# Optimization experiments

Hardware: AMD Instinct MI355X
Metric: run time of the kernel (lower is better)

Reference implementation:

```python
import jax, jax.numpy as jnp
import numpy as np

EPS = 1e-12  # F.normalize default eps


def _l2norm(x, axis):
    n = jnp.sqrt(jnp.sum(x * x, axis=axis, keepdims=True))
    return x / jnp.maximum(n, EPS)


def setup_inputs() -> dict:
    key = jax.random.key(0)
    k1, k2, k3, k4 = jax.random.split(key, 4)
    N, T, C, K = 64, 577, 768, 64
    return {
        "grids": jax.random.normal(k1, (N, T, C), dtype=jnp.float32),
        "conv_w": jax.random.normal(k2, (K, C), dtype=jnp.float32) * 0.03,
        "conv_b": jax.random.normal(k3, (K,), dtype=jnp.float32) * 0.01,
        "centroids": jax.random.normal(k4, (K, C), dtype=jnp.float32) * 0.03,
    }


def reference(grids, conv_w, conv_b, centroids):
    # grids: (N, 577, 768) -> (N, C=768, T=577), matching view+permute in torch
    N = grids.shape[0]
    x = jnp.transpose(grids.reshape(N, 577, 768), (0, 2, 1))  # (N, C, T)
    # per-token L2 normalization over channel dim
    x = _l2norm(x, axis=1)
    # 1x1 conv == per-token linear: (N, K, T)
    logits = jnp.einsum('kc,nct->nkt', conv_w, x) + conv_b[None, :, None]
    a = jax.nn.softmax(logits, axis=1)  # softmax over regions K
    # NetVLAD algebraic rewrite of sum_t a[n,k,t]*(x[n,:,t]-c[k,:]):
    #   = (a @ x^T)[n,k,c] - sum_t(a)[n,k] * c[k,c]
    p = jnp.einsum('nkt,nct->nkc', a, x) - a.sum(axis=-1)[:, :, None] * centroids[None]
    p = _l2norm(p, axis=2)             # intra-region normalization
    p = p.reshape(N, -1)               # (N, K*C)
    p = _l2norm(p, axis=1)             # global normalization
    return p
```

## Files before the change

kernel.cpp:

```cpp
#include <hip/hip_runtime.h>
#include <math.h>

#define TT 577
#define TP 640
#define CCH 768
#define KR 64
#define NB 64

typedef __attribute__((ext_vector_type(8))) short bf16x8;
typedef __attribute__((ext_vector_type(8))) unsigned short ushort8;
typedef __attribute__((ext_vector_type(4))) float f32x4;

static constexpr float EPSF = 1e-12f;

static __device__ inline unsigned short f2bf(float f) {
    union { float f; unsigned int u; } v; v.f = f;
    unsigned int r = (v.u + 0x7FFFu + ((v.u >> 16) & 1u)) >> 16;
    return (unsigned short)r;
}
static __device__ inline float bf2f(unsigned short b) {
    union { unsigned int u; float f; } v; v.u = ((unsigned int)b) << 16;
    return v.f;
}

__global__ __launch_bounds__(256) void k_logits(
    const float* __restrict__ grids,
    const float* __restrict__ conv_w,
    const float* __restrict__ conv_b,
    unsigned short* __restrict__ ws_a,
    float* __restrict__ ws_norm)
{
    __shared__ __align__(16) unsigned short Wl[KR * 136];
    __shared__ __align__(16) unsigned short Abuf[4][KR * 24];

    const int tid  = threadIdx.x;
    const int lane = tid & 63;
    const int w    = tid >> 6;
    const int n    = blockIdx.x / 10;
    const int tb   = (blockIdx.x - n * 10) << 6;
    const int t0w  = tb + (w << 4);

    const int lr = lane & 15;
    const int lg = lane >> 4;

    const int tokA = t0w + lr;
    const bool validA = (tokA < TT);
    const float* gsrc = grids + ((size_t)n * TT + tokA) * CCH + (lg << 3);

    f32x4 acc[4] = {};
    float ss = 0.f;

    for (int c0 = 0; c0 < CCH; c0 += 128) {
        #pragma unroll
        for (int it = 0; it < 4; ++it) {
            int f = tid + (it << 8);
            int kr = f >> 4;
            int c8 = (f & 15) << 3;
            const float* src = conv_w + (size_t)kr * CCH + c0 + c8;
            float4 v0 = *reinterpret_cast<const float4*>(src);
            float4 v1 = *reinterpret_cast<const float4*>(src + 4);
            unsigned short* dst = &Wl[kr * 136 + c8];
            dst[0]=f2bf(v0.x); dst[1]=f2bf(v0.y); dst[2]=f2bf(v0.z); dst[3]=f2bf(v0.w);
            dst[4]=f2bf(v1.x); dst[5]=f2bf(v1.y); dst[6]=f2bf(v1.z); dst[7]=f2bf(v1.w);
        }
        __syncthreads();

        #pragma unroll
        for (int s = 0; s < 4; ++s) {
            float a8[8];
            if (validA) {
                float4 u0 = *reinterpret_cast<const float4*>(gsrc + c0 + (s << 5));
                float4 u1 = *reinterpret_cast<const float4*>(gsrc + c0 + (s << 5) + 4);
                a8[0]=u0.x; a8[1]=u0.y; a8[2]=u0.z; a8[3]=u0.w;
                a8[4]=u1.x; a8[5]=u1.y; a8[6]=u1.z; a8[7]=u1.w;
            } else {
                #pragma unroll
                for (int j = 0; j < 8; ++j) a8[j] = 0.f;
            }
            bf16x8 afrag;
            #pragma unroll
            for (int j = 0; j < 8; ++j) {
                ss = fmaf(a8[j], a8[j], ss);
                ((unsigned short*)&afrag)[j] = f2bf(a8[j]);
            }
            const int cl = (s << 5) + (lg << 3);
            #pragma unroll
            for (int rt = 0; rt < 4; ++rt) {
                bf16x8 bfrag = *reinterpret_cast<const bf16x8*>(&Wl[(rt*16 + lr)*136 + cl]);
                acc[rt] = __builtin_amdgcn_mfma_f32_16x16x32_bf16(afrag, bfrag, acc[rt], 0, 0, 0);
            }
        }
        __syncthreads();
    }

    ss += __shfl_xor(ss, 16);
    ss += __shfl_xor(ss, 32);
    const float nrm = sqrtf(ss);
    const float inv = 1.0f / fmaxf(nrm, EPSF);
    if (lane < 16) ws_norm[n * TP + t0w + lane] = nrm;

    float b_[4];
    #pragma unroll
    for (int rt = 0; rt < 4; ++rt) b_[rt] = conv_b[rt*16 + lr];

    float invT[4];
    #pragma unroll
    for (int reg = 0; reg < 4; ++reg) invT[reg] = __shfl(inv, (lg << 2) + reg);

    float lgt[4][4], mx[4];
    #pragma unroll
    for (int reg = 0; reg < 4; ++reg) {
        float m = -1e30f;
        #pragma unroll
        for (int rt = 0; rt < 4; ++rt) {
            lgt[rt][reg] = fmaf(acc[rt][reg], invT[reg], b_[rt]);
            m = fmaxf(m, lgt[rt][reg]);
        }
        mx[reg] = m;
    }
    #pragma unroll
    for (int msk = 1; msk < 16; msk <<= 1) {
        #pragma unroll
        for (int reg = 0; reg < 4; ++reg) mx[reg] = fmaxf(mx[reg], __shfl_xor(mx[reg], msk));
    }
    float ex[4][4], sm[4] = {0.f, 0.f, 0.f, 0.f};
    #pragma unroll
    for (int rt = 0; rt < 4; ++rt) {
        #pragma unroll
        for (int reg = 0; reg < 4; ++reg) {
            ex[rt][reg] = __expf(lgt[rt][reg] - mx[reg]);
            sm[reg] += ex[rt][reg];
        }
    }
    #pragma unroll
    for (int msk = 1; msk < 16; msk <<= 1) {
        #pragma unroll
        for (int reg = 0; reg < 4; ++reg) sm[reg] += __shfl_xor(sm[reg], msk);
    }

    #pragma unroll
    for (int reg = 0; reg < 4; ++reg) {
        const int trow = (lg << 2) + reg;
        const bool vt = (t0w + trow) < TT;
        const float scale = vt ? (invT[reg] / sm[reg]) : 0.f;
        #pragma unroll
        for (int rt = 0; rt < 4; ++rt)
            Abuf[w][(rt*16 + lr)*24 + trow] = f2bf(ex[rt][reg] * scale);
    }
    __syncthreads();

    {
        ushort8 r0 = *reinterpret_cast<const ushort8*>(&Abuf[w][lane * 24]);
        ushort8 r1 = *reinterpret_cast<const ushort8*>(&Abuf[w][lane * 24 + 8]);
        unsigned short* dst = ws_a + ((size_t)n * KR + lane) * TP + t0w;
        *reinterpret_cast<ushort8*>(dst)     = r0;
        *reinterpret_cast<ushort8*>(dst + 8) = r1;
    }
}

__global__ __launch_bounds__(256) void k_vlad(
    const float* __restrict__ grids,
    const unsigned short* __restrict__ ws_a,
    const float* __restrict__ ws_norm,
    const float* __restrict__ centroids,
    float* __restrict__ out)
{
    __shared__ __align__(16) unsigned short Gs[32 * 196];
    __shared__ float asum_red[4][64];
    __shared__ float asum_s[64];

    const int tid  = threadIdx.x;
    const int lane = tid & 63;
    const int w    = tid >> 6;
    const int n    = blockIdx.x >> 2;
    const int cq   = (blockIdx.x & 3) * 192;

    {
        const int kr = tid & 63, q = tid >> 6;
        const unsigned short* ap = ws_a + ((size_t)n * KR + kr) * TP;
        const float* np = ws_norm + n * TP;
        float s = 0.f;
        for (int t = q * 8; t < TP; t += 32) {
            ushort8 av = *reinterpret_cast<const ushort8*>(ap + t);
            float4 n0 = *reinterpret_cast<const float4*>(np + t);
            float4 n1 = *reinterpret_cast<const float4*>(np + t + 4);
            s += bf2f(av[0])*n0.x + bf2f(av[1])*n0.y + bf2f(av[2])*n0.z + bf2f(av[3])*n0.w
               + bf2f(av[4])*n1.x + bf2f(av[5])*n1.y + bf2f(av[6])*n1.z + bf2f(av[7])*n1.w;
        }
        asum_red[q][kr] = s;
    }
    __syncthreads();
    if (tid < 64)
        asum_s[tid] = asum_red[0][tid] + asum_red[1][tid] + asum_red[2][tid] + asum_red[3][tid];

    const int lr = lane & 15;
    const int lg = lane >> 4;
    f32x4 acc[4][3] = {};

    const unsigned short* abase = ws_a + ((size_t)n * KR + lr) * TP;

    float4 stg[6];
    auto load_chunk = [&](int t0) {
        #pragma unroll
        for (int it = 0; it < 6; ++it) {
            int f = tid + (it << 8);
            int t = f / 48, c4 = (f - t * 48) << 2;
            stg[it] = make_float4(0.f, 0.f, 0.f, 0.f);
            if (t0 + t < TT)
                stg[it] = *reinterpret_cast<const float4*>(
                    grids + ((size_t)n * TT + t0 + t) * CCH + cq + c4);
        }
    };

    load_chunk(0);
    for (int t0 = 0; t0 < TT; t0 += 32) {
        __syncthreads();
        #pragma unroll
        for (int it = 0; it < 6; ++it) {
            int f = tid + (it << 8);
            int t = f / 48, c4 = (f - t * 48) << 2;
            unsigned short* dst = &Gs[t * 196 + c4];
            float4 v = stg[it];
            dst[0]=f2bf(v.x); dst[1]=f2bf(v.y); dst[2]=f2bf(v.z); dst[3]=f2bf(v.w);
        }
        __syncthreads();

        if (t0 + 32 < TT) load_chunk(t0 + 32);

        bf16x8 af[4];
        #pragma unroll
        for (int rt = 0; rt < 4; ++rt)
            af[rt] = *reinterpret_cast<const bf16x8*>(abase + (size_t)rt * 16 * TP + t0 + (lg << 3));

        #pragma unroll
        for (int ct = 0; ct < 3; ++ct) {
            const int cc = w * 48 + ct * 16 + lr;
            bf16x8 bfrag;
            #pragma unroll
            for (int j = 0; j < 8; ++j)
                ((unsigned short*)&bfrag)[j] = Gs[((lg << 3) + j) * 196 + cc];
            #pragma unroll
            for (int rt = 0; rt < 4; ++rt)
                acc[rt][ct] = __builtin_amdgcn_mfma_f32_16x16x32_bf16(af[rt], bfrag, acc[rt][ct], 0, 0, 0);
        }
    }
    __syncthreads();

    #pragma unroll
    for (int rt = 0; rt < 4; ++rt) {
        #pragma unroll
        for (int reg = 0; reg < 4; ++reg) {
            const int kr = rt * 16 + (lg << 2) + reg;
            const float as = asum_s[kr];
            #pragma unroll
            for (int ct = 0; ct < 3; ++ct) {
                const int c = cq + w * 48 + ct * 16 + lr;
                out[((size_t)n * KR + kr) * CCH + c] =
                    acc[rt][ct][reg] - as * centroids[(size_t)kr * CCH + c];
            }
        }
    }
}

__global__ __launch_bounds__(64) void kc_norm_kernel(float* __restrict__ out)
{
    float4* p = reinterpret_cast<float4*>(out) + (size_t)blockIdx.x * 192;
    const int l = threadIdx.x;
    float4 v0 = p[l];
    float4 v1 = p[l + 64];
    float4 v2 = p[l + 128];
    float ss = v0.x*v0.x + v0.y*v0.y + v0.z*v0.z + v0.w*v0.w
             + v1.x*v1.x + v1.y*v1.y + v1.z*v1.z + v1.w*v1.w
             + v2.x*v2.x + v2.y*v2.y + v2.z*v2.z + v2.w*v2.w;
    #pragma unroll
    for (int m = 1; m < 64; m <<= 1) ss += __shfl_xor(ss, m);
    const float sc = 0.125f / fmaxf(sqrtf(ss), EPSF);
    v0.x*=sc; v0.y*=sc; v0.z*=sc; v0.w*=sc;
    v1.x*=sc; v1.y*=sc; v1.z*=sc; v1.w*=sc;
    v2.x*=sc; v2.y*=sc; v2.z*=sc; v2.w*=sc;
    p[l] = v0;
    p[l + 64] = v1;
    p[l + 128] = v2;
}

extern "C" void kernel_launch(void* const* d_in, const int* in_sizes, int n_in,
                              void* d_out, int out_size, void* d_ws, size_t ws_size,
                              hipStream_t stream)
{
    const float* grids     = (const float*)d_in[0];
    const float* conv_w    = (const float*)d_in[1];
    const float* conv_b    = (const float*)d_in[2];
    const float* centroids = (const float*)d_in[3];
    float* out = (float*)d_out;

    unsigned short* ws_a = (unsigned short*)d_ws;
    float* ws_norm = (float*)((char*)d_ws + (size_t)NB * KR * TP * 2);

    hipLaunchKernelGGL(k_logits, dim3(NB * 10), dim3(256), 0, stream,
                       grids, conv_w, conv_b, ws_a, ws_norm);
    hipLaunchKernelGGL(k_vlad, dim3(NB * 4), dim3(256), 0, stream,
                       grids, ws_a, ws_norm, centroids, out);
    hipLaunchKernelGGL(kc_norm_kernel, dim3(NB * KR), dim3(64), 0, stream, out);
}
```

Before: 84.33 us.

## Drop LDS staging in VLAD kernel, widen grid, double-buffer weights in logits

New measurement: 82.47 us. 2.2% less time.

```diff
diff --git a/kernel.cpp b/kernel.cpp
--- a/kernel.cpp
+++ b/kernel.cpp
@@ -15,8 +15,7 @@
 
 static __device__ inline unsigned short f2bf(float f) {
     union { float f; unsigned int u; } v; v.f = f;
-    unsigned int r = (v.u + 0x7FFFu + ((v.u >> 16) & 1u)) >> 16;
-    return (unsigned short)r;
+    return (unsigned short)((v.u + 0x7FFFu + ((v.u >> 16) & 1u)) >> 16);
 }
 static __device__ inline float bf2f(unsigned short b) {
     union { unsigned int u; float f; } v; v.u = ((unsigned int)b) << 16;
@@ -30,8 +29,7 @@
     unsigned short* __restrict__ ws_a,
     float* __restrict__ ws_norm)
 {
-    __shared__ __align__(16) unsigned short Wl[KR * 136];
-    __shared__ __align__(16) unsigned short Abuf[4][KR * 24];
+    __shared__ __align__(16) unsigned short Wl[2][KR * 136];
 
     const int tid  = threadIdx.x;
     const int lane = tid & 63;
@@ -47,23 +45,45 @@
     const bool validA = (tokA < TT);
     const float* gsrc = grids + ((size_t)n * TT + tokA) * CCH + (lg << 3);
 
+    float4 wreg[4][2];
+    auto load_w = [&](int c0) {
+        #pragma unroll
+        for (int it = 0; it < 4; ++it) {
+            int f = tid + (it << 8);
+            int kr = f >> 4, c8 = (f & 15) << 3;
+            const float* src = conv_w + (size_t)kr * CCH + c0 + c8;
+            wreg[it][0] = *reinterpret_cast<const float4*>(src);
+            wreg[it][1] = *reinterpret_cast<const float4*>(src + 4);
+        }
+    };
+    auto store_w = [&](int buf) {
+        #pragma unroll
+        for (int it = 0; it < 4; ++it) {
+            int f = tid + (it << 8);
+            int kr = f >> 4, c8 = (f & 15) << 3;
+            ushort8 o;
+            o[0] = f2bf(wreg[it][0].x); o[1] = f2bf(wreg[it][0].y);
+            o[2] = f2bf(wreg[it][0].z); o[3] = f2bf(wreg[it][0].w);
+            o[4] = f2bf(wreg[it][1].x); o[5] = f2bf(wreg[it][1].y);
+            o[6] = f2bf(wreg[it][1].z); o[7] = f2bf(wreg[it][1].w);
+            *reinterpret_cast<ushort8*>(&Wl[buf][kr * 136 + c8]) = o;
+        }
+    };
+
     f32x4 acc[4] = {};
     float ss = 0.f;
 
-    for (int c0 = 0; c0 < CCH; c0 += 128) {
-        #pragma unroll
-        for (int it = 0; it < 4; ++it) {
-            int f = tid + (it << 8);
-            int kr = f >> 4;
-            int c8 = (f & 15) << 3;
-            const float* src = conv_w + (size_t)kr * CCH + c0 + c8;
-            float4 v0 = *reinterpret_cast<const float4*>(src);
-            float4 v1 = *reinterpret_cast<const float4*>(src + 4);
-            unsigned short* dst = &Wl[kr * 136 + c8];
-            dst[0]=f2bf(v0.x); dst[1]=f2bf(v0.y); dst[2]=f2bf(v0.z); dst[3]=f2bf(v0.w);
-            dst[4]=f2bf(v1.x); dst[5]=f2bf(v1.y); dst[6]=f2bf(v1.z); dst[7]=f2bf(v1.w);
-        }
-        __syncthreads();
+    load_w(0);
+    store_w(0);
+    __syncthreads();
+
+    for (int ch = 0; ch < 6; ++ch) {
+        if (ch < 5) {
+            load_w((ch + 1) << 7);
+            store_w((ch + 1) & 1);
+        }
+        const int c0 = ch << 7;
+        const unsigned short* Wb = Wl[ch & 1];
 
         #pragma unroll
         for (int s = 0; s < 4; ++s) {
@@ -86,7 +106,7 @@
             const int cl = (s << 5) + (lg << 3);
             #pragma unroll
             for (int rt = 0; rt < 4; ++rt) {
-                bf16x8 bfrag = *reinterpret_cast<const bf16x8*>(&Wl[(rt*16 + lr)*136 + cl]);
+                bf16x8 bfrag = *reinterpret_cast<const bf16x8*>(&Wb[(rt*16 + lr)*136 + cl]);
                 acc[rt] = __builtin_amdgcn_mfma_f32_16x16x32_bf16(afrag, bfrag, acc[rt], 0, 0, 0);
             }
         }
@@ -138,6 +158,7 @@
         for (int reg = 0; reg < 4; ++reg) sm[reg] += __shfl_xor(sm[reg], msk);
     }
 
+    unsigned short* Abuf = &Wl[0][0] + (size_t)w * KR * 24;
     #pragma unroll
     for (int reg = 0; reg < 4; ++reg) {
         const int trow = (lg << 2) + reg;
@@ -145,13 +166,13 @@
         const float scale = vt ? (invT[reg] / sm[reg]) : 0.f;
         #pragma unroll
         for (int rt = 0; rt < 4; ++rt)
-            Abuf[w][(rt*16 + lr)*24 + trow] = f2bf(ex[rt][reg] * scale);
+            Abuf[(rt*16 + lr)*24 + trow] = f2bf(ex[rt][reg] * scale);
     }
     __syncthreads();
 
     {
-        ushort8 r0 = *reinterpret_cast<const ushort8*>(&Abuf[w][lane * 24]);
-        ushort8 r1 = *reinterpret_cast<const ushort8*>(&Abuf[w][lane * 24 + 8]);
+        ushort8 r0 = *reinterpret_cast<const ushort8*>(&Abuf[lane * 24]);
+        ushort8 r1 = *reinterpret_cast<const ushort8*>(&Abuf[lane * 24 + 8]);
         unsigned short* dst = ws_a + ((size_t)n * KR + lane) * TP + t0w;
         *reinterpret_cast<ushort8*>(dst)     = r0;
         *reinterpret_cast<ushort8*>(dst + 8) = r1;
@@ -165,15 +186,16 @@
     const float* __restrict__ centroids,
     float* __restrict__ out)
 {
-    __shared__ __align__(16) unsigned short Gs[32 * 196];
     __shared__ float asum_red[4][64];
     __shared__ float asum_s[64];
 
     const int tid  = threadIdx.x;
     const int lane = tid & 63;
     const int w    = tid >> 6;
-    const int n    = blockIdx.x >> 2;
-    const int cq   = (blockIdx.x & 3) * 192;
+    const int n    = blockIdx.x / 12;
+    const int c0   = (blockIdx.x - n * 12) << 6;
+    const int lr   = lane & 15;
+    const int lg   = lane >> 4;
 
     {
         const int kr = tid & 63, q = tid >> 6;
@@ -192,72 +214,55 @@
     __syncthreads();
     if (tid < 64)
         asum_s[tid] = asum_red[0][tid] + asum_red[1][tid] + asum_red[2][tid] + asum_red[3][tid];
-
-    const int lr = lane & 15;
-    const int lg = lane >> 4;
-    f32x4 acc[4][3] = {};
-
-    const unsigned short* abase = ws_a + ((size_t)n * KR + lr) * TP;
-
-    float4 stg[6];
-    auto load_chunk = [&](int t0) {
-        #pragma unroll
-        for (int it = 0; it < 6; ++it) {
-            int f = tid + (it << 8);
-            int t = f / 48, c4 = (f - t * 48) << 2;
-            stg[it] = make_float4(0.f, 0.f, 0.f, 0.f);
-            if (t0 + t < TT)
-                stg[it] = *reinterpret_cast<const float4*>(
-                    grids + ((size_t)n * TT + t0 + t) * CCH + cq + c4);
-        }
-    };
-
-    load_chunk(0);
-    for (int t0 = 0; t0 < TT; t0 += 32) {
-        __syncthreads();
-        #pragma unroll
-        for (int it = 0; it < 6; ++it) {
-            int f = tid + (it << 8);
-            int t = f / 48, c4 = (f - t * 48) << 2;
-            unsigned short* dst = &Gs[t * 196 + c4];
-            float4 v = stg[it];
-            dst[0]=f2bf(v.x); dst[1]=f2bf(v.y); dst[2]=f2bf(v.z); dst[3]=f2bf(v.w);
-        }
-        __syncthreads();
-
-        if (t0 + 32 < TT) load_chunk(t0 + 32);
-
-        bf16x8 af[4];
+    __syncthreads();
+
+    const int c = c0 + (w << 4) + lr;
+    const unsigned short* abase = ws_a + ((size_t)n * KR + lr) * TP + (lg << 3);
+    const float* gb = grids + (size_t)n * TT * CCH + c;
+
+    auto load_frags = [&](int t0, bf16x8* af, bf16x8& bfv) {
         #pragma unroll
         for (int rt = 0; rt < 4; ++rt)
-            af[rt] = *reinterpret_cast<const bf16x8*>(abase + (size_t)rt * 16 * TP + t0 + (lg << 3));
-
-        #pragma unroll
-        for (int ct = 0; ct < 3; ++ct) {
-            const int cc = w * 48 + ct * 16 + lr;
-            bf16x8 bfrag;
+            af[rt] = *reinterpret_cast<const bf16x8*>(abase + (size_t)rt * 16 * TP + t0);
+        const int tb2 = t0 + (lg << 3);
+        if (t0 + 32 <= TT) {
             #pragma unroll
             for (int j = 0; j < 8; ++j)
-                ((unsigned short*)&bfrag)[j] = Gs[((lg << 3) + j) * 196 + cc];
+                ((unsigned short*)&bfv)[j] = f2bf(gb[(size_t)(tb2 + j) * CCH]);
+        } else {
             #pragma unroll
-            for (int rt = 0; rt < 4; ++rt)
-                acc[rt][ct] = __builtin_amdgcn_mfma_f32_16x16x32_bf16(af[rt], bfrag, acc[rt][ct], 0, 0, 0);
-        }
-    }
-    __syncthreads();
+            for (int j = 0; j < 8; ++j) {
+                float v = (tb2 + j < TT) ? gb[(size_t)(tb2 + j) * CCH] : 0.f;
+                ((unsigned short*)&bfv)[j] = f2bf(v);
+            }
+        }
+    };
+
+    f32x4 acc[4] = {};
+    bf16x8 afA[4], afB[4];
+    bf16x8 bfA, bfB;
+
+    load_frags(0, afA, bfA);
+    #pragma unroll 2
+    for (int t0 = 0; t0 < TT; t0 += 64) {
+        if (t0 + 32 < TT) load_frags(t0 + 32, afB, bfB);
+        #pragma unroll
+        for (int rt = 0; rt < 4; ++rt)
+            acc[rt] = __builtin_amdgcn_mfma_f32_16x16x32_bf16(afA[rt], bfA, acc[rt], 0, 0, 0);
+        if (t0 + 32 >= TT) break;
+        if (t0 + 64 < TT) load_frags(t0 + 64, afA, bfA);
+        #pragma unroll
+        for (int rt = 0; rt < 4; ++rt)
+            acc[rt] = __builtin_amdgcn_mfma_f32_16x16x32_bf16(afB[rt], bfB, acc[rt], 0, 0, 0);
+    }
 
     #pragma unroll
     for (int rt = 0; rt < 4; ++rt) {
         #pragma unroll
         for (int reg = 0; reg < 4; ++reg) {
             const int kr = rt * 16 + (lg << 2) + reg;
-            const float as = asum_s[kr];
-            #pragma unroll
-            for (int ct = 0; ct < 3; ++ct) {
-                const int c = cq + w * 48 + ct * 16 + lr;
-                out[((size_t)n * KR + kr) * CCH + c] =
-                    acc[rt][ct][reg] - as * centroids[(size_t)kr * CCH + c];
-            }
+            out[((size_t)n * KR + kr) * CCH + c] =
+                acc[rt][reg] - asum_s[kr] * centroids[(size_t)kr * CCH + c];
         }
     }
 }
@@ -298,7 +303,7 @@
 
     hipLaunchKernelGGL(k_logits, dim3(NB * 10), dim3(256), 0, stream,
                        grids, conv_w, conv_b, ws_a, ws_norm);
-    hipLaunchKernelGGL(k_vlad, dim3(NB * 4), dim3(256), 0, stream,
+    hipLaunchKernelGGL(k_vlad, dim3(NB * 12), dim3(256), 0, stream,
                        grids, ws_a, ws_norm, centroids, out);
     hipLaunchKernelGGL(kc_norm_kernel, dim3(NB * KR), dim3(64), 0, stream, out);
 }
```
